# Kernel tuning notes

Measured on AMD Instinct MI355X. Metric: run time of the kernel, lower is better.

The kernel has to match this reference:

```python
import jax, jax.numpy as jnp
import numpy as np

DIM = 768
NUM_HEADS = 12
HEAD_DIM = DIM // NUM_HEADS
SCALE = HEAD_DIM ** -0.5


def setup_inputs() -> dict:
    key = jax.random.key(0)
    k1, k2, k3 = jax.random.split(key, 3)
    B, N = 4, 2048
    x = jax.random.normal(k1, (B, N, DIM), dtype=jnp.float32)
    Wqkv = jax.random.normal(k2, (DIM, 3 * DIM), dtype=jnp.float32) * (DIM ** -0.5)
    Wproj = jax.random.normal(k3, (DIM, DIM), dtype=jnp.float32) * (DIM ** -0.5)
    bproj = jnp.zeros((DIM,), dtype=jnp.float32)
    return {"x": x, "Wqkv": Wqkv, "Wproj": Wproj, "bproj": bproj}


def reference(x, Wqkv, Wproj, bproj):
    B, N, C = x.shape
    # qkv: [B, N, 3, H, D] -> split into q, k, v each [B, H, N, D]
    qkv = (x @ Wqkv).reshape(B, N, 3, NUM_HEADS, HEAD_DIM)
    qkv = jnp.transpose(qkv, (2, 0, 3, 1, 4))
    q, k, v = qkv[0], qkv[1], qkv[2]
    attn = jnp.einsum("bhnd,bhmd->bhnm", q, k) * SCALE
    attn = jax.nn.softmax(attn, axis=-1)  # dropout p=0 -> identity
    out = jnp.einsum("bhnm,bhmd->bhnd", attn, v)
    out = jnp.transpose(out, (0, 2, 1, 3)).reshape(B, N, C)
    return out @ Wproj + bproj
```

## Files before the change

### kernel.cpp

```cpp
#include <hip/hip_runtime.h>
#include <math.h>

typedef __bf16 bf16;
typedef __attribute__((ext_vector_type(8))) __bf16 bf16x8;
typedef __attribute__((ext_vector_type(4))) __bf16 bf16x4;
typedef __attribute__((ext_vector_type(4))) float f32x4;

#define NHEADS 12
#define HDIM 64
#define BATCH 4
#define SEQ 2048
#define CDIM 768
#define MTOK (BATCH * SEQ)
#define PERPART ((size_t)MTOK * CDIM)
#define NBH (BATCH * NHEADS)
#define NKB (SEQ / 64)

#define KSCALE 0.18033688011112042f
#define SHIFT 11.54156032f

__device__ static inline void load_lds_16(const void* g, void* l)
{
    __builtin_amdgcn_global_load_lds(
        (const __attribute__((address_space(1))) unsigned int*)g,
        (__attribute__((address_space(3))) unsigned int*)l, 16, 0, 0);
}

__global__ __launch_bounds__(256)
void prep(const float* __restrict__ x, const float* __restrict__ Wqkv,
          const float* __restrict__ Wproj,
          bf16* __restrict__ xb, bf16* __restrict__ wqt, bf16* __restrict__ wpt)
{
    __shared__ bf16 T[64][65];
    const int bid = blockIdx.x;
    const int t   = threadIdx.x;

    if (bid < 3072) {
        const size_t i = ((size_t)bid * 256 + t) * 8;
        const float4 v0 = *(const float4*)(x + i);
        const float4 v1 = *(const float4*)(x + i + 4);
        alignas(16) bf16 o[8];
        o[0] = (bf16)v0.x; o[1] = (bf16)v0.y; o[2] = (bf16)v0.z; o[3] = (bf16)v0.w;
        o[4] = (bf16)v1.x; o[5] = (bf16)v1.y; o[6] = (bf16)v1.z; o[7] = (bf16)v1.w;
        *(uint4*)(xb + i) = *(const uint4*)o;
        return;
    }

    const float* in; bf16* outp; int C, bx, by;
    if (bid < 3072 + 432) {
        const int b2 = bid - 3072;
        in = Wqkv; outp = wqt; C = 3 * CDIM; bx = b2 % 36; by = b2 / 36;
    } else {
        const int b2 = bid - 3504;
        in = Wproj; outp = wpt; C = CDIM;    bx = b2 % 12; by = b2 / 12;
    }
    const int r0 = by * 64, c0 = bx * 64;
    const int ir = t >> 2, ic = (t & 3) * 16;
    #pragma unroll
    for (int e = 0; e < 16; ++e)
        T[ir][ic + e] = (bf16)in[(size_t)(r0 + ir) * C + c0 + ic + e];
    __syncthreads();
    const int oc = t >> 2, orr = (t & 3) * 16;
    alignas(16) bf16 tmp[16];
    #pragma unroll
    for (int e = 0; e < 16; ++e)
        tmp[e] = T[orr + e][oc];
    bf16* dst = outp + (size_t)(c0 + oc) * CDIM + r0 + orr;
    *(uint4*)dst       = *(const uint4*)tmp;
    *(uint4*)(dst + 8) = *(const uint4*)(tmp + 8);
}

template<int BN, int MODE>
__global__ __launch_bounds__(256, 3)
void gemm128(const bf16* __restrict__ A, const bf16* __restrict__ Bt,
             const float* __restrict__ bias,
             bf16* __restrict__ qb, bf16* __restrict__ kb, bf16* __restrict__ vtb,
             float* __restrict__ outf)
{
    constexpr int NT = BN / 32;
    __shared__ bf16 As[128 * 64];
    __shared__ bf16 Bs[BN * 64];

    const int t    = threadIdx.x;
    const int w    = t >> 6, lane = t & 63;
    const int ln   = lane & 15, quad = lane >> 4;
    const int wr   = w >> 1, wc = w & 1;
    const int m0   = blockIdx.x * 128, n0 = blockIdx.y * BN;

    f32x4 acc[4][NT] = {};

    for (int k0 = 0; k0 < CDIM; k0 += 64) {
        #pragma unroll
        for (int i = 0; i < 4; ++i) {
            const int S   = w * 256 + i * 64 + lane;
            const int row = S >> 3, g = (S & 7) ^ (row & 7);
            load_lds_16(A + (size_t)(m0 + row) * CDIM + k0 + g * 8,
                        &As[(w * 4 + i) * 512]);
        }
        #pragma unroll
        for (int i = 0; i < NT; ++i) {
            const int S   = w * (BN * 2) + i * 64 + lane;
            const int row = S >> 3, g = (S & 7) ^ (row & 7);
            load_lds_16(Bt + (size_t)(n0 + row) * CDIM + k0 + g * 8,
                        &Bs[(w * NT + i) * 512]);
        }
        __syncthreads();

        #pragma unroll
        for (int kk = 0; kk < 2; ++kk) {
            bf16x8 af[4], bf_[NT];
            #pragma unroll
            for (int mt = 0; mt < 4; ++mt) {
                const int row = wr * 64 + mt * 16 + ln;
                af[mt] = *(const bf16x8*)&As[row * 64 + ((kk * 4 + quad) ^ (row & 7)) * 8];
            }
            #pragma unroll
            for (int nt = 0; nt < NT; ++nt) {
                const int row = wc * (BN / 2) + nt * 16 + ln;
                bf_[nt] = *(const bf16x8*)&Bs[row * 64 + ((kk * 4 + quad) ^ (row & 7)) * 8];
            }
            #pragma unroll
            for (int mt = 0; mt < 4; ++mt)
                #pragma unroll
                for (int nt = 0; nt < NT; ++nt)
                    acc[mt][nt] = __builtin_amdgcn_mfma_f32_16x16x32_bf16(
                        af[mt], bf_[nt], acc[mt][nt], 0, 0, 0);
        }
        __syncthreads();
    }

    #pragma unroll
    for (int nt = 0; nt < NT; ++nt) {
        const int c = n0 + wc * (BN / 2) + nt * 16 + ln;
        if constexpr (MODE == 0) {
            const int p = c / CDIM, rem = c - p * CDIM;
            const int h = rem >> 6, d = rem & 63;
            #pragma unroll
            for (int mt = 0; mt < 4; ++mt) {
                const int row0 = m0 + wr * 64 + mt * 16 + quad * 4;
                const int b = row0 >> 11, nn = row0 & 2047;
                if (p == 0) {
                    bf16* dst = qb + ((size_t)(b * NHEADS + h) * SEQ + nn) * HDIM + d;
                    #pragma unroll
                    for (int r = 0; r < 4; ++r) dst[r * HDIM] = (bf16)acc[mt][nt][r];
                } else if (p == 1) {
                    bf16* dst = kb + ((size_t)(b * NHEADS + h) * SEQ + nn) * HDIM + d;
                    #pragma unroll
                    for (int r = 0; r < 4; ++r) dst[r * HDIM] = (bf16)(acc[mt][nt][r] * KSCALE);
                } else {
                    alignas(8) bf16 pk[4];
                    #pragma unroll
                    for (int r = 0; r < 4; ++r) pk[r] = (bf16)acc[mt][nt][r];
                    const int nn2 = (nn & ~31) + ((nn >> 2) & 3) * 8 + ((nn >> 4) & 1) * 4;
                    *(uint2*)(vtb + ((size_t)(b * NHEADS + h) * HDIM + d) * SEQ + nn2) =
                        *(const uint2*)pk;
                }
            }
        } else {
            const float bv = bias[c];
            #pragma unroll
            for (int mt = 0; mt < 4; ++mt) {
                const int row0 = m0 + wr * 64 + mt * 16 + quad * 4;
                #pragma unroll
                for (int r = 0; r < 4; ++r)
                    outf[(size_t)(row0 + r) * CDIM + c] = acc[mt][nt][r] + bv;
            }
        }
    }
}

__global__ __launch_bounds__(256, 4)
void attn_kernel(const bf16* __restrict__ Qg, const bf16* __restrict__ Kg,
                 const bf16* __restrict__ Vtg, bf16* __restrict__ ao)
{
    __shared__ bf16 Ks[2][64 * 64];
    __shared__ bf16 Vs[2][64 * 64];

    const int virt = (blockIdx.x & 7) * 96 + (blockIdx.x >> 3);
    const int xq   = virt & 15;
    const int bh   = virt >> 4;

    const int t    = threadIdx.x;
    const int w    = t >> 6, lane = t & 63;
    const int ln   = lane & 15, quad = lane >> 4;
    const int q0   = xq * 128;

    const bf16* Qb = Qg  + (size_t)bh * SEQ * HDIM;
    const bf16* Kb = Kg  + (size_t)bh * SEQ * HDIM;
    const bf16* Vb = Vtg + (size_t)bh * HDIM * SEQ;

    bf16x8 qf[2][2];
    #pragma unroll
    for (int qt = 0; qt < 2; ++qt)
        #pragma unroll
        for (int kk = 0; kk < 2; ++kk) {
            const int row = w * 32 + qt * 16 + ln;
            qf[qt][kk] = *(const bf16x8*)(Qb + (size_t)(q0 + row) * HDIM
                                          + (kk * 4 + quad) * 8);
        }

    #pragma unroll
    for (int i = 0; i < 2; ++i) {
        const int S = w * 128 + i * 64 + lane;
        const int row = S >> 3, g = (S & 7) ^ (row & 7);
        load_lds_16(Kb + (size_t)row * HDIM + g * 8, &Ks[0][(w * 2 + i) * 512]);
        load_lds_16(Vb + (size_t)row * SEQ + g * 8,  &Vs[0][(w * 2 + i) * 512]);
    }
    __syncthreads();

    bf16x8 ones;
    #pragma unroll
    for (int e = 0; e < 8; ++e) ones[e] = (bf16)1.0f;

    f32x4 o_acc[2][4] = {};
    f32x4 racc[2] = {};

    for (int kb = 0; kb < NKB; ++kb) {
        if (kb + 1 < NKB) {
            const int nb   = (kb + 1) & 1;
            const int kpos = (kb + 1) * 64;
            #pragma unroll
            for (int i = 0; i < 2; ++i) {
                const int S = w * 128 + i * 64 + lane;
                const int row = S >> 3, g = (S & 7) ^ (row & 7);
                load_lds_16(Kb + (size_t)(kpos + row) * HDIM + g * 8,
                            &Ks[nb][(w * 2 + i) * 512]);
                load_lds_16(Vb + (size_t)row * SEQ + kpos + g * 8,
                            &Vs[nb][(w * 2 + i) * 512]);
            }
        }

        const bf16* Ksb = Ks[kb & 1];
        const bf16* Vsb = Vs[kb & 1];

        #pragma unroll
        for (int p = 0; p < 2; ++p) {
            union { bf16x8 v8; bf16x4 v4[2]; } pf8[2];
            #pragma unroll
            for (int sub = 0; sub < 2; ++sub) {
                const int mt = p * 2 + sub;
                bf16x8 ka[2];
                #pragma unroll
                for (int kk = 0; kk < 2; ++kk) {
                    const int row = mt * 16 + ln;
                    const int g = (kk * 4 + quad) ^ (row & 7);
                    ka[kk] = *(const bf16x8*)&Ksb[row * 64 + g * 8];
                }
                #pragma unroll
                for (int qt = 0; qt < 2; ++qt) {
                    f32x4 a = {-SHIFT, -SHIFT, -SHIFT, -SHIFT};
                    a = __builtin_amdgcn_mfma_f32_16x16x32_bf16(ka[0], qf[qt][0], a, 0, 0, 0);
                    a = __builtin_amdgcn_mfma_f32_16x16x32_bf16(ka[1], qf[qt][1], a, 0, 0, 0);
                    bf16x4 pb = { (bf16)__builtin_amdgcn_exp2f(a[0]),
                                  (bf16)__builtin_amdgcn_exp2f(a[1]),
                                  (bf16)__builtin_amdgcn_exp2f(a[2]),
                                  (bf16)__builtin_amdgcn_exp2f(a[3]) };
                    pf8[qt].v4[sub] = pb;
                }
            }
            __builtin_amdgcn_s_setprio(1);
            #pragma unroll
            for (int qt = 0; qt < 2; ++qt)
                racc[qt] = __builtin_amdgcn_mfma_f32_16x16x32_bf16(
                    pf8[qt].v8, ones, racc[qt], 0, 0, 0);
            #pragma unroll
            for (int dt = 0; dt < 4; ++dt) {
                const int row = dt * 16 + ln;
                const int g = (p * 4 + quad) ^ (row & 7);
                const bf16x8 vvv = *(const bf16x8*)&Vsb[row * 64 + g * 8];
                #pragma unroll
                for (int qt = 0; qt < 2; ++qt)
                    o_acc[qt][dt] = __builtin_amdgcn_mfma_f32_16x16x32_bf16(
                        pf8[qt].v8, vvv, o_acc[qt][dt], 0, 0, 0);
            }
            __builtin_amdgcn_s_setprio(0);
        }
        __syncthreads();
    }

    const int b = bh / NHEADS, h = bh - b * NHEADS;
    bf16* Ao = ao + (size_t)b * SEQ * CDIM + h * HDIM;
    #pragma unroll
    for (int qt = 0; qt < 2; ++qt) {
        float inv[4];
        #pragma unroll
        for (int r = 0; r < 4; ++r) inv[r] = 1.0f / racc[qt][r];
        #pragma unroll
        for (int dt = 0; dt < 4; ++dt) {
            const int d = dt * 16 + ln;
            #pragma unroll
            for (int r = 0; r < 4; ++r) {
                const int q = q0 + w * 32 + qt * 16 + quad * 4 + r;
                Ao[(size_t)q * CDIM + d] = (bf16)(o_acc[qt][dt][r] * inv[r]);
            }
        }
    }
}

extern "C" void kernel_launch(void* const* d_in, const int* in_sizes, int n_in,
                              void* d_out, int out_size, void* d_ws, size_t ws_size,
                              hipStream_t stream)
{
    const float* x     = (const float*)d_in[0];
    const float* Wqkv  = (const float*)d_in[1];
    const float* Wproj = (const float*)d_in[2];
    const float* bproj = (const float*)d_in[3];
    float* out = (float*)d_out;

    bf16* ws   = (bf16*)d_ws;
    bf16* xb   = ws;
    bf16* wqt  = xb  + PERPART;
    bf16* wpt  = wqt + (size_t)3 * CDIM * CDIM;
    bf16* q    = wpt + (size_t)CDIM * CDIM;
    bf16* k    = q   + PERPART;
    bf16* vt   = k   + PERPART;
    bf16* ao   = vt  + PERPART;

    prep<<<dim3(3072 + 432 + 144), 256, 0, stream>>>(x, Wqkv, Wproj, xb, wqt, wpt);

    gemm128<192, 0><<<dim3(MTOK / 128, 3 * CDIM / 192), 256, 0, stream>>>(
        xb, wqt, nullptr, q, k, vt, nullptr);
    attn_kernel<<<dim3(16 * NBH), 256, 0, stream>>>(q, k, vt, ao);
    gemm128<96, 1><<<dim3(MTOK / 128, CDIM / 96), 256, 0, stream>>>(
        ao, wpt, bproj, nullptr, nullptr, nullptr, out);
}
```

Measured before the change: 185.6 us.

## Double-buffer QKV GEMM LDS tiles with K-step of 32 and async prefetch

Splits the templated GEMM into separate QKV and projection kernels. The QKV GEMM now uses two LDS buffers with a K-step of 32, prefetching the next tile via global_load_lds while MFMAs run on the current one, which needs only one barrier per step. The aim is to hide global load latency behind compute. In exchange there are twice as many iterations and barriers, and each step issues fewer MFMAs, so the barrier overhead per step is relatively larger.

```diff
diff --git a/kernel.cpp b/kernel.cpp
--- a/kernel.cpp
+++ b/kernel.cpp
@@ -70,16 +70,14 @@
     *(uint4*)(dst + 8) = *(const uint4*)(tmp + 8);
 }
 
-template<int BN, int MODE>
 __global__ __launch_bounds__(256, 3)
-void gemm128(const bf16* __restrict__ A, const bf16* __restrict__ Bt,
-             const float* __restrict__ bias,
-             bf16* __restrict__ qb, bf16* __restrict__ kb, bf16* __restrict__ vtb,
-             float* __restrict__ outf)
-{
-    constexpr int NT = BN / 32;
-    __shared__ bf16 As[128 * 64];
-    __shared__ bf16 Bs[BN * 64];
+void gemm_qkv(const bf16* __restrict__ A, const bf16* __restrict__ Bt,
+              bf16* __restrict__ qb, bf16* __restrict__ kb,
+              bf16* __restrict__ vtb)
+{
+    constexpr int BN = 192, NT = 6;
+    __shared__ bf16 As[2][128 * 32];
+    __shared__ bf16 Bs[2][BN * 32];
 
     const int t    = threadIdx.x;
     const int w    = t >> 6, lane = t & 63;
@@ -87,6 +85,111 @@
     const int wr   = w >> 1, wc = w & 1;
     const int m0   = blockIdx.x * 128, n0 = blockIdx.y * BN;
 
+    int arow[2], ag[2], brow[3], bg[3];
+    #pragma unroll
+    for (int i = 0; i < 2; ++i) {
+        const int S = w * 128 + i * 64 + lane;
+        arow[i] = S >> 2; ag[i] = (S & 3) ^ (arow[i] & 3);
+    }
+    #pragma unroll
+    for (int i = 0; i < 3; ++i) {
+        const int S = w * 192 + i * 64 + lane;
+        brow[i] = S >> 2; bg[i] = (S & 3) ^ (brow[i] & 3);
+    }
+
+    f32x4 acc[4][NT] = {};
+
+    #pragma unroll
+    for (int i = 0; i < 2; ++i)
+        load_lds_16(A + (size_t)(m0 + arow[i]) * CDIM + ag[i] * 8,
+                    &As[0][(w * 2 + i) * 512]);
+    #pragma unroll
+    for (int i = 0; i < 3; ++i)
+        load_lds_16(Bt + (size_t)(n0 + brow[i]) * CDIM + bg[i] * 8,
+                    &Bs[0][(w * 3 + i) * 512]);
+    __syncthreads();
+
+    const int NSTEP = CDIM / 32;
+    for (int s = 0; s < NSTEP; ++s) {
+        if (s + 1 < NSTEP) {
+            const int nb = (s + 1) & 1, k0 = (s + 1) * 32;
+            #pragma unroll
+            for (int i = 0; i < 2; ++i)
+                load_lds_16(A + (size_t)(m0 + arow[i]) * CDIM + k0 + ag[i] * 8,
+                            &As[nb][(w * 2 + i) * 512]);
+            #pragma unroll
+            for (int i = 0; i < 3; ++i)
+                load_lds_16(Bt + (size_t)(n0 + brow[i]) * CDIM + k0 + bg[i] * 8,
+                            &Bs[nb][(w * 3 + i) * 512]);
+        }
+
+        const bf16* Asb = As[s & 1];
+        const bf16* Bsb = Bs[s & 1];
+
+        bf16x8 af[4], bf_[NT];
+        #pragma unroll
+        for (int mt = 0; mt < 4; ++mt) {
+            const int row = wr * 64 + mt * 16 + ln;
+            af[mt] = *(const bf16x8*)&Asb[row * 32 + (quad ^ (row & 3)) * 8];
+        }
+        #pragma unroll
+        for (int nt = 0; nt < NT; ++nt) {
+            const int row = wc * (BN / 2) + nt * 16 + ln;
+            bf_[nt] = *(const bf16x8*)&Bsb[row * 32 + (quad ^ (row & 3)) * 8];
+        }
+        #pragma unroll
+        for (int mt = 0; mt < 4; ++mt)
+            #pragma unroll
+            for (int nt = 0; nt < NT; ++nt)
+                acc[mt][nt] = __builtin_amdgcn_mfma_f32_16x16x32_bf16(
+                    af[mt], bf_[nt], acc[mt][nt], 0, 0, 0);
+
+        __syncthreads();
+    }
+
+    #pragma unroll
+    for (int nt = 0; nt < NT; ++nt) {
+        const int c = n0 + wc * (BN / 2) + nt * 16 + ln;
+        const int p = c / CDIM, rem = c - p * CDIM;
+        const int h = rem >> 6, d = rem & 63;
+        #pragma unroll
+        for (int mt = 0; mt < 4; ++mt) {
+            const int row0 = m0 + wr * 64 + mt * 16 + quad * 4;
+            const int b = row0 >> 11, nn = row0 & 2047;
+            if (p == 0) {
+                bf16* dst = qb + ((size_t)(b * NHEADS + h) * SEQ + nn) * HDIM + d;
+                #pragma unroll
+                for (int r = 0; r < 4; ++r) dst[r * HDIM] = (bf16)acc[mt][nt][r];
+            } else if (p == 1) {
+                bf16* dst = kb + ((size_t)(b * NHEADS + h) * SEQ + nn) * HDIM + d;
+                #pragma unroll
+                for (int r = 0; r < 4; ++r) dst[r * HDIM] = (bf16)(acc[mt][nt][r] * KSCALE);
+            } else {
+                alignas(8) bf16 pk[4];
+                #pragma unroll
+                for (int r = 0; r < 4; ++r) pk[r] = (bf16)acc[mt][nt][r];
+                const int nn2 = (nn & ~31) + ((nn >> 2) & 3) * 8 + ((nn >> 4) & 1) * 4;
+                *(uint2*)(vtb + ((size_t)(b * NHEADS + h) * HDIM + d) * SEQ + nn2) =
+                    *(const uint2*)pk;
+            }
+        }
+    }
+}
+
+__global__ __launch_bounds__(256, 3)
+void gemm_proj(const bf16* __restrict__ A, const bf16* __restrict__ Bt,
+               const float* __restrict__ bias, float* __restrict__ outf)
+{
+    constexpr int BN = 96, NT = 3;
+    __shared__ bf16 As[128 * 64];
+    __shared__ bf16 Bs[BN * 64];
+
+    const int t    = threadIdx.x;
+    const int w    = t >> 6, lane = t & 63;
+    const int ln   = lane & 15, quad = lane >> 4;
+    const int wr   = w >> 1, wc = w & 1;
+    const int m0   = blockIdx.x * 128, n0 = blockIdx.y * BN;
+
     f32x4 acc[4][NT] = {};
 
     for (int k0 = 0; k0 < CDIM; k0 += 64) {
@@ -132,39 +235,13 @@
     #pragma unroll
     for (int nt = 0; nt < NT; ++nt) {
         const int c = n0 + wc * (BN / 2) + nt * 16 + ln;
-        if constexpr (MODE == 0) {
-            const int p = c / CDIM, rem = c - p * CDIM;
-            const int h = rem >> 6, d = rem & 63;
-            #pragma unroll
-            for (int mt = 0; mt < 4; ++mt) {
-                const int row0 = m0 + wr * 64 + mt * 16 + quad * 4;
-                const int b = row0 >> 11, nn = row0 & 2047;
-                if (p == 0) {
-                    bf16* dst = qb + ((size_t)(b * NHEADS + h) * SEQ + nn) * HDIM + d;
-                    #pragma unroll
-                    for (int r = 0; r < 4; ++r) dst[r * HDIM] = (bf16)acc[mt][nt][r];
-                } else if (p == 1) {
-                    bf16* dst = kb + ((size_t)(b * NHEADS + h) * SEQ + nn) * HDIM + d;
-                    #pragma unroll
-                    for (int r = 0; r < 4; ++r) dst[r * HDIM] = (bf16)(acc[mt][nt][r] * KSCALE);
-                } else {
-                    alignas(8) bf16 pk[4];
-                    #pragma unroll
-                    for (int r = 0; r < 4; ++r) pk[r] = (bf16)acc[mt][nt][r];
-                    const int nn2 = (nn & ~31) + ((nn >> 2) & 3) * 8 + ((nn >> 4) & 1) * 4;
-                    *(uint2*)(vtb + ((size_t)(b * NHEADS + h) * HDIM + d) * SEQ + nn2) =
-                        *(const uint2*)pk;
-                }
-            }
-        } else {
-            const float bv = bias[c];
-            #pragma unroll
-            for (int mt = 0; mt < 4; ++mt) {
-                const int row0 = m0 + wr * 64 + mt * 16 + quad * 4;
-                #pragma unroll
-                for (int r = 0; r < 4; ++r)
-                    outf[(size_t)(row0 + r) * CDIM + c] = acc[mt][nt][r] + bv;
-            }
+        const float bv = bias[c];
+        #pragma unroll
+        for (int mt = 0; mt < 4; ++mt) {
+            const int row0 = m0 + wr * 64 + mt * 16 + quad * 4;
+            #pragma unroll
+            for (int r = 0; r < 4; ++r)
+                outf[(size_t)(row0 + r) * CDIM + c] = acc[mt][nt][r] + bv;
         }
     }
 }
@@ -318,9 +395,9 @@
 
     prep<<<dim3(3072 + 432 + 144), 256, 0, stream>>>(x, Wqkv, Wproj, xb, wqt, wpt);
 
-    gemm128<192, 0><<<dim3(MTOK / 128, 3 * CDIM / 192), 256, 0, stream>>>(
-        xb, wqt, nullptr, q, k, vt, nullptr);
+    gemm_qkv<<<dim3(MTOK / 128, 3 * CDIM / 192), 256, 0, stream>>>(
+        xb, wqt, q, k, vt);
     attn_kernel<<<dim3(16 * NBH), 256, 0, stream>>>(q, k, vt, ao);
-    gemm128<96, 1><<<dim3(MTOK / 128, CDIM / 96), 256, 0, stream>>>(
-        ao, wpt, bproj, nullptr, nullptr, nullptr, out);
-}
+    gemm_proj<<<dim3(MTOK / 128, CDIM / 96), 256, 0, stream>>>(
+        ao, wpt, bproj, out);
+}
```

After: 191.0 us. 1.03x slower.
